# Kernel tuning notes

Measured on AMD Instinct MI355X. Metric: run time of the kernel, lower is better.

## Reference

```python
import jax, jax.numpy as jnp
import numpy as np

EPS = 1e-5

def _bn(x, g, b):
    # training-mode batchnorm over all axes except the last (channel)
    axes = tuple(range(x.ndim - 1))
    m = x.mean(axis=axes, keepdims=True)
    v = x.var(axis=axes, keepdims=True)
    return (x - m) * jax.lax.rsqrt(v + EPS) * g + b

def setup_inputs() -> dict:
    key = jax.random.key(0)
    ks = jax.random.split(key, 9)
    B, N = 4, 4096
    def w(i, shape, fan_in):
        return jax.random.normal(ks[i], shape, jnp.float32) * np.float32(1.0 / np.sqrt(fan_in))
    return {
        "x": jax.random.normal(ks[0], (B, 3, N), jnp.float32),
        "Wq": w(1, (64, 3), 3),
        "Wkv": w(2, (128, 3), 3),
        "Wp1": w(3, (64, 3), 3),
        "Wp2": w(4, (64, 64), 64),
        "Wa": w(5, (64, 64), 64),
        "Wc1": w(6, (64, 64), 64),
        "Wsk": w(7, (64, 6), 6),
        "Wga": w(8, (64, 128), 128),
        "g_p": jnp.ones(64, jnp.float32), "b_p": jnp.zeros(64, jnp.float32),
        "g_a": jnp.ones(64, jnp.float32), "b_a": jnp.zeros(64, jnp.float32),
        "g_c": jnp.ones(64, jnp.float32), "b_c": jnp.zeros(64, jnp.float32),
        "g_sk": jnp.ones(64, jnp.float32), "b_sk": jnp.zeros(64, jnp.float32),
        "g_ga": jnp.ones(64, jnp.float32), "b_ga": jnp.zeros(64, jnp.float32),
        "k": 32,
    }

def reference(x, Wq, Wkv, Wp1, Wp2, Wa, Wc1, Wsk, Wga,
              g_p, b_p, g_a, b_a, g_c, b_c, g_sk, b_sk, g_ga, b_ga, k):
    # x: [B, 3, N] point cloud
    xt = jnp.transpose(x, (0, 2, 1))                      # [B, N, 3]
    B = xt.shape[0]
    # --- KNN neighbor grouping (irregular gather) ---
    sq = jnp.sum(xt * xt, axis=-1)                        # [B, N]
    dist = sq[:, :, None] + sq[:, None, :] - 2.0 * jnp.einsum('bnc,bmc->bnm', xt, xt)
    _, idx = jax.lax.top_k(-dist, k)                      # [B, N, k]
    grouped = xt[jnp.arange(B)[:, None, None], idx]       # [B, N, k, 3]
    rel = grouped - xt[:, :, None, :]                     # relative coords
    # --- local self-attention (1x1 conv QKV + position encoding) ---
    q = jnp.einsum('bnc,dc->bnd', xt, Wq)[:, :, None, :]  # [B, N, 1, 64]
    kv = jnp.einsum('bnkc,dc->bnkd', rel, Wkv)            # [B, N, k, 128]
    kf, vf = kv[..., :64], kv[..., 64:]
    pos = jnp.einsum('bnkd,ed->bnke',
                     jax.nn.relu(_bn(jnp.einsum('bnkc,dc->bnkd', rel, Wp1), g_p, b_p)),
                     Wp2)                                 # [B, N, k, 64]
    logits = jax.nn.relu(_bn(jnp.einsum('bnkd,ed->bnke', q - kf + pos, Wa), g_a, b_a))
    attn = jax.nn.softmax(logits, axis=2)                 # softmax over k neighbors
    agg = jnp.sum(attn * (vf + pos), axis=2)              # [B, N, 64]
    # --- pointnet conv-BN head + skip + fusion ---
    h = jax.nn.relu(_bn(jnp.einsum('bnd,ed->bne', agg, Wc1), g_c, b_c))
    nb_max = jnp.max(grouped, axis=2)                     # [B, N, 3] max-pool over neighbors
    sk = jax.nn.relu(_bn(jnp.einsum('bnc,dc->bnd',
                                    jnp.concatenate([xt, nb_max], axis=-1), Wsk), g_sk, b_sk))
    out = jax.nn.relu(_bn(jnp.einsum('bnc,dc->bnd',
                                     jnp.concatenate([h, sk], axis=-1), Wga), g_ga, b_ga))
    return jnp.transpose(out, (0, 2, 1))                  # [B, 64, N]
```

## Files before the change

### kernel.cpp

```cpp
#include <hip/hip_runtime.h>

#define NBATCH 4
#define NPTS   4096
#define NP     (NBATCH*NPTS)
#define KK     32
#define INF    __builtin_inff()

static const size_t OFF_PTS  = 0;
static const size_t OFF_IDX  = 65536;
static const size_t OFF_TSK  = 589824;
static const size_t OFF_TC   = 1638400;
static const size_t OFF_TGA  = 2686976;
static const size_t OFF_PREL = 3735552;
static const size_t OFF_PSK  = 3735568;
static const size_t OFF_PTA  = 3735696;
static const size_t OFF_PTC  = 3735824;
static const size_t OFF_PTGA = 3735952;
static const size_t OFF_AFF  = 3736080;

typedef __bf16 bf16x8  __attribute__((ext_vector_type(8)));
typedef float  floatx16 __attribute__((ext_vector_type(16)));
#define MFMA32(a,b,c) __builtin_amdgcn_mfma_f32_32x32x16_bf16(a, b, c, 0, 0, 0)

union F8 { bf16x8 v; unsigned short us[8]; uint4 q4; };

__device__ __forceinline__ unsigned short bfbits(float f) {
  unsigned u = __float_as_uint(f);
  return (unsigned short)((u + 0x7FFFu + ((u >> 16) & 1u)) >> 16);
}
__device__ __forceinline__ floatx16 zero16() {
  floatx16 v;
#pragma unroll
  for (int i = 0; i < 16; ++i) v[i] = 0.f;
  return v;
}
__device__ __forceinline__ float wsum(float v) {
#pragma unroll
  for (int o = 32; o; o >>= 1) v += __shfl_xor(v, o, 64);
  return v;
}
__device__ __forceinline__ int isum(int v) {
#pragma unroll
  for (int o = 32; o; o >>= 1) v += __shfl_xor(v, o);
  return v;
}

__global__ __launch_bounds__(256,1) void k_prep(const float* __restrict__ x, float4* __restrict__ pts,
                                                float* __restrict__ pta, float* __restrict__ ptc,
                                                float* __restrict__ ptga, float* __restrict__ prel9,
                                                float* __restrict__ psk128) {
  if (blockIdx.x == 0) {
    if (threadIdx.x < 128) {
      pta[threadIdx.x] = 0.f; ptc[threadIdx.x] = 0.f; ptga[threadIdx.x] = 0.f;
      psk128[threadIdx.x] = 0.f;
    }
    if (threadIdx.x < 16) prel9[threadIdx.x] = 0.f;
  }
  int g = blockIdx.x * 256 + threadIdx.x;
  int b = g / NPTS, n = g % NPTS;
  float vx = x[(b*3+0)*NPTS + n];
  float vy = x[(b*3+1)*NPTS + n];
  float vz = x[(b*3+2)*NPTS + n];
  pts[g] = make_float4(vx, vy, vz, vx*vx + vy*vy + vz*vz);
}

__global__ __launch_bounds__(256) void k_knn(const float4* __restrict__ pts, int* __restrict__ idx,
                                             const float* __restrict__ Wsk, float* __restrict__ tsk,
                                             float* __restrict__ prel9, float* __restrict__ psk128) {
  __shared__ int ocnt[4];
  __shared__ int lsel[128];
  __shared__ float rsum[9], psum[64], pss[64];
  const int tid  = threadIdx.x;
  const int w    = tid >> 6;
  const int lane = tid & 63;
  if (tid < 9)  rsum[tid] = 0.f;
  if (tid < 64) { psum[tid] = 0.f; pss[tid] = 0.f; }
  __syncthreads();
  const int n = blockIdx.x * 4 + w;
  const int batch = n >> 12;
  const float4* base = pts + batch * NPTS;
  const float4 me = pts[n];
  const float wk0 = Wsk[lane*6+0], wk1 = Wsk[lane*6+1], wk2 = Wsk[lane*6+2],
              wk3 = Wsk[lane*6+3], wk4 = Wsk[lane*6+4], wk5 = Wsk[lane*6+5];

  unsigned t0 = 0xFFFFFFFFu, t1 = 0xFFFFFFFFu, t2 = 0xFFFFFFFFu,
           t3 = 0xFFFFFFFFu, t4 = 0xFFFFFFFFu, t5 = 0xFFFFFFFFu;
#pragma unroll 4
  for (int j = 0; j < 64; ++j) {
    float4 p = base[j*64 + lane];
    float dot = fmaf(me.x, p.x, fmaf(me.y, p.y, me.z * p.z));
    float d = fmaxf(fmaf(-2.f, dot, me.w + p.w), 0.f);
    unsigned m = __float_as_uint(d), x;
    x = min(t0, m); m = max(t0, m); t0 = x;
    x = min(t1, m); m = max(t1, m); t1 = x;
    x = min(t2, m); m = max(t2, m); t2 = x;
    x = min(t3, m); m = max(t3, m); t3 = x;
    x = min(t4, m); m = max(t4, m); t4 = x;
    t5 = min(t5, m);
  }

  unsigned glo = t0, ghi = t5;
#pragma unroll
  for (int o = 32; o; o >>= 1) {
    glo = min(glo, (unsigned)__shfl_xor((int)glo, o));
    ghi = max(ghi, (unsigned)__shfl_xor((int)ghi, o));
  }

  unsigned lo = glo, hi = ghi, tau = ghi;
  bool exact = false;
  while (lo < hi) {
    unsigned mid = lo + ((hi - lo) >> 1);
    int c = (t0 <= mid) + (t1 <= mid) + (t2 <= mid) +
            (t3 <= mid) + (t4 <= mid) + (t5 <= mid);
    c = isum(c);
    if (c == 32) { tau = mid; exact = true; break; }
    if (c > 32) hi = mid; else lo = mid + 1;
  }
  if (!exact) tau = lo;

  if (__ballot(t5 <= tau) != 0ull) {
    lo = glo; hi = tau; exact = false;
    while (lo < hi) {
      unsigned mid = lo + ((hi - lo) >> 1);
      int c = 0;
      for (int j = 0; j < 64; ++j) {
        float4 p = base[j*64 + lane];
        float dot = fmaf(me.x, p.x, fmaf(me.y, p.y, me.z * p.z));
        float d = fmaxf(fmaf(-2.f, dot, me.w + p.w), 0.f);
        c += (__float_as_uint(d) <= mid) ? 1 : 0;
      }
      c = isum(c);
      if (c == 32) { tau = mid; exact = true; break; }
      if (c > 32) hi = mid; else lo = mid + 1;
    }
    if (!exact) tau = lo;
  }

  if (lane == 0) ocnt[w] = 0;
  int* op = idx + n * KK;
  unsigned long long em = 0;
#pragma unroll 4
  for (int j = 0; j < 64; ++j) {
    float4 p = base[j*64 + lane];
    float dot = fmaf(me.x, p.x, fmaf(me.y, p.y, me.z * p.z));
    float d = fmaxf(fmaf(-2.f, dot, me.w + p.w), 0.f);
    unsigned k = __float_as_uint(d);
    bool take = exact ? (k <= tau) : (k < tau);
    if (take) {
      int s = atomicAdd(&ocnt[w], 1);
      int m = j*64 + lane;
      if (s < KK) { op[s] = m; lsel[w*32 + s] = m; }
    }
    if (k == tau) em |= 1ull << j;
  }
  if (!exact) {
    int n1 = ocnt[w];
    int need = KK - n1;
    for (int f = 0; f < need; ++f) {
      int myj = em ? (int)__builtin_ctzll(em) : 64;
      int mym = (myj < 64) ? (myj*64 + lane) : 0x7FFFFFFF;
      int g = mym;
#pragma unroll
      for (int o = 32; o; o >>= 1) g = min(g, __shfl_xor(g, o));
      if (mym == g && myj < 64) { em &= em - 1; op[n1 + f] = mym; lsel[w*32 + n1 + f] = mym; }
    }
  }

  int mi = lsel[w*32 + (lane & 31)];
  float4 p = base[mi];
  bool act = lane < 32;
  float r0 = act ? p.x - me.x : 0.f;
  float r1 = act ? p.y - me.y : 0.f;
  float r2 = act ? p.z - me.z : 0.f;
  float vals[9] = { r0, r1, r2, r0*r0, r0*r1, r0*r2, r1*r1, r1*r2, r2*r2 };
#pragma unroll
  for (int t = 0; t < 9; ++t) {
    float rs = wsum(vals[t]);
    if (lane == 0) atomicAdd(&rsum[t], rs);
  }
  float nx = act ? p.x : -INF, ny = act ? p.y : -INF, nz = act ? p.z : -INF;
#pragma unroll
  for (int o = 32; o; o >>= 1) {
    nx = fmaxf(nx, __shfl_xor(nx, o));
    ny = fmaxf(ny, __shfl_xor(ny, o));
    nz = fmaxf(nz, __shfl_xor(nz, o));
  }
  float ts = fmaf(me.x, wk0, fmaf(me.y, wk1, fmaf(me.z, wk2,
             fmaf(nx, wk3, fmaf(ny, wk4, nz * wk5)))));
  tsk[n*64 + lane] = ts;
  atomicAdd(&psum[lane], ts);
  atomicAdd(&pss[lane], ts * ts);
  __syncthreads();
  if (tid < 9)  atomicAdd(&prel9[tid], rsum[tid]);
  if (tid < 64) atomicAdd(&psk128[tid], psum[tid]);
  else if (tid < 128) atomicAdd(&psk128[tid], pss[tid - 64]);
}

__global__ __launch_bounds__(64,1) void k_fin1(const float* __restrict__ prel9, const float* __restrict__ psk128,
                                               const float* __restrict__ Wp1,
                                               const float* __restrict__ g_p, const float* __restrict__ b_p,
                                               const float* __restrict__ g_sk, const float* __restrict__ b_sk,
                                               float* __restrict__ aff) {
  int d = threadIdx.x;
  double C = (double)NP * (double)KK;
  double mr0 = prel9[0]/C, mr1 = prel9[1]/C, mr2 = prel9[2]/C;
  double e00 = prel9[3]/C, e01 = prel9[4]/C, e02 = prel9[5]/C;
  double e11 = prel9[6]/C, e12 = prel9[7]/C, e22 = prel9[8]/C;
  double w0 = Wp1[d*3+0], w1 = Wp1[d*3+1], w2 = Wp1[d*3+2];
  double mu  = w0*mr0 + w1*mr1 + w2*mr2;
  double ex2 = w0*w0*e00 + w1*w1*e11 + w2*w2*e22 + 2.0*(w0*w1*e01 + w0*w2*e02 + w1*w2*e12);
  double var = ex2 - mu*mu;
  double sc  = (double)g_p[d] / sqrt(var + 1e-5);
  aff[0*64 + d] = (float)sc;
  aff[1*64 + d] = (float)((double)b_p[d] - mu*sc);
  double mean = (double)psk128[d] / (double)NP;
  double v2   = (double)psk128[64+d] / (double)NP - mean*mean;
  double sc4  = (double)g_sk[d] / sqrt(v2 + 1e-5);
  aff[6*64 + d] = (float)sc4;
  aff[7*64 + d] = (float)((double)b_sk[d] - mean*sc4);
}

__global__ __launch_bounds__(64,1) void k_fin2(const float* __restrict__ st, double C,
                                               const float* __restrict__ g, const float* __restrict__ b,
                                               float* __restrict__ s_out, float* __restrict__ o_out) {
  int d = threadIdx.x;
  double mean = (double)st[d] / C;
  double var  = (double)st[64 + d] / C - mean*mean;
  double sc   = (double)g[d] / sqrt(var + 1e-5);
  s_out[d] = (float)sc;
  o_out[d] = (float)((double)b[d] - mean*sc);
}

template<int MODE>
__global__ __launch_bounds__(256,1) void k_entry(const float4* __restrict__ pts, const int* __restrict__ idx,
                                                 const float* __restrict__ Wq, const float* __restrict__ Wkv,
                                                 const float* __restrict__ Wp1, const float* __restrict__ Wp2,
                                                 const float* __restrict__ Wa, const float* __restrict__ Wc1,
                                                 const float* __restrict__ aff, float* __restrict__ pstats,
                                                 float* __restrict__ tc) {
  __shared__ __align__(16) unsigned short ybuf[4][32][72];
  __shared__ __align__(16) float aggbuf[4][64];
  __shared__ float psum[64], pss[64];
  if (threadIdx.x < 64) { psum[threadIdx.x] = 0.f; pss[threadIdx.x] = 0.f; }
  __syncthreads();
  const int lane = threadIdx.x & 63;
  const int w    = threadIdx.x >> 6;
  const int c    = lane & 31;
  const int q5   = lane >> 5;

  F8 B0[2];
#pragma unroll
  for (int nt = 0; nt < 2; ++nt)
#pragma unroll
    for (int t = 0; t < 8; ++t)
      B0[nt].us[t] = (q5 == 0 && t < 3) ? bfbits(Wp1[(nt*32+c)*3 + t]) : (unsigned short)0;

  F8 Bs[4][2], B2[4][2];
#pragma unroll
  for (int kt = 0; kt < 4; ++kt)
#pragma unroll
    for (int h = 0; h < 2; ++h) {
      const float* p2 = Wp2 + (h*32+c)*64 + kt*16 + q5*8;
      float4 a = *(const float4*)p2, b = *(const float4*)(p2 + 4);
      Bs[kt][h].us[0]=bfbits(a.x); Bs[kt][h].us[1]=bfbits(a.y); Bs[kt][h].us[2]=bfbits(a.z); Bs[kt][h].us[3]=bfbits(a.w);
      Bs[kt][h].us[4]=bfbits(b.x); Bs[kt][h].us[5]=bfbits(b.y); Bs[kt][h].us[6]=bfbits(b.z); Bs[kt][h].us[7]=bfbits(b.w);
      const float* pa = Wa + (h*32+c)*64 + kt*16 + q5*8;
      float4 e = *(const float4*)pa, f = *(const float4*)(pa + 4);
      B2[kt][h].us[0]=bfbits(e.x); B2[kt][h].us[1]=bfbits(e.y); B2[kt][h].us[2]=bfbits(e.z); B2[kt][h].us[3]=bfbits(e.w);
      B2[kt][h].us[4]=bfbits(f.x); B2[kt][h].us[5]=bfbits(f.y); B2[kt][h].us[6]=bfbits(f.z); B2[kt][h].us[7]=bfbits(f.w);
    }

  F8 Bk4[4];
#pragma unroll
  for (int nt = 0; nt < 4; ++nt) {
    if (MODE == 0 && nt >= 2) { for (int t = 0; t < 8; ++t) Bk4[nt].us[t] = 0; continue; }
    int e = (nt & 1)*32 + c;
#pragma unroll
    for (int t = 0; t < 8; ++t)
      Bk4[nt].us[t] = (q5 == 0 && t < 3)
        ? bfbits(nt < 2 ? -Wkv[e*3 + t] : Wkv[(64+e)*3 + t]) : (unsigned short)0;
  }

  const float s1a = aff[c],      o1a = aff[64+c];
  const float s1b = aff[32+c],   o1b = aff[96+c];
  float s2a = 0.f, o2a = 0.f, s2b = 0.f, o2b = 0.f;
  if (MODE == 1) { s2a = aff[128+c]; o2a = aff[192+c]; s2b = aff[160+c]; o2b = aff[224+c]; }
  const float wqa0 = Wq[c*3+0],      wqa1 = Wq[c*3+1],      wqa2 = Wq[c*3+2];
  const float wqb0 = Wq[(32+c)*3+0], wqb1 = Wq[(32+c)*3+1], wqb2 = Wq[(32+c)*3+2];

  const int wave_id = blockIdx.x * 4 + w;
  const int n0 = wave_id * 8;
  const int batch = n0 >> 12;
  const float4* base = pts + batch * NPTS;

  for (int pi = 0; pi < 8; ++pi) {
    const int n = n0 + pi;
    const float4 me = pts[n];
    const int nb = idx[n*KK + c];
    const float4 pp = base[nb];
    const float r0 = pp.x - me.x, r1 = pp.y - me.y, r2 = pp.z - me.z;
    F8 relA;
#pragma unroll
    for (int t = 0; t < 8; ++t) relA.us[t] = 0;
    if (q5 == 0) { relA.us[0] = bfbits(r0); relA.us[1] = bfbits(r1); relA.us[2] = bfbits(r2); }

    const floatx16 z = zero16();
    floatx16 y0 = MFMA32(relA.v, B0[0].v, z);
    floatx16 y1 = MFMA32(relA.v, B0[1].v, z);
#pragma unroll
    for (int r = 0; r < 16; ++r) {
      int row = (r & 3) + 8*(r >> 2) + 4*q5;
      ybuf[w][row][c]      = bfbits(fmaxf(fmaf(y0[r], s1a, o1a), 0.f));
      ybuf[w][row][32 + c] = bfbits(fmaxf(fmaf(y1[r], s1b, o1b), 0.f));
    }
    F8 Ay[4];
#pragma unroll
    for (int kt = 0; kt < 4; ++kt) Ay[kt].q4 = *(const uint4*)&ybuf[w][c][kt*16 + q5*8];

    floatx16 Cp0 = z, Cp1 = z;
#pragma unroll
    for (int kt = 0; kt < 4; ++kt) {
      Cp0 = MFMA32(Ay[kt].v, Bs[kt][0].v, Cp0);
      Cp1 = MFMA32(Ay[kt].v, Bs[kt][1].v, Cp1);
    }
    floatx16 Cu0 = MFMA32(relA.v, Bk4[0].v, Cp0);
    floatx16 Cu1 = MFMA32(relA.v, Bk4[1].v, Cp1);
    if (MODE == 1) {
      Cp0 = MFMA32(relA.v, Bk4[2].v, Cp0);
      Cp1 = MFMA32(relA.v, Bk4[3].v, Cp1);
    }
    const float qa = fmaf(me.x, wqa0, fmaf(me.y, wqa1, me.z * wqa2));
    const float qb = fmaf(me.x, wqb0, fmaf(me.y, wqb1, me.z * wqb2));
#pragma unroll
    for (int r = 0; r < 16; ++r) {
      int row = (r & 3) + 8*(r >> 2) + 4*q5;
      ybuf[w][row][c]      = bfbits(Cu0[r] + qa);
      ybuf[w][row][32 + c] = bfbits(Cu1[r] + qb);
    }
    F8 Au[4];
#pragma unroll
    for (int kt = 0; kt < 4; ++kt) Au[kt].q4 = *(const uint4*)&ybuf[w][c][kt*16 + q5*8];
    floatx16 Ct0 = z, Ct1 = z;
#pragma unroll
    for (int kt = 0; kt < 4; ++kt) {
      Ct0 = MFMA32(Au[kt].v, B2[kt][0].v, Ct0);
      Ct1 = MFMA32(Au[kt].v, B2[kt][1].v, Ct1);
    }

    if (MODE == 0) {
      float sa = 0.f, qqa = 0.f, sb = 0.f, qqb = 0.f;
#pragma unroll
      for (int r = 0; r < 16; ++r) {
        sa += Ct0[r]; qqa = fmaf(Ct0[r], Ct0[r], qqa);
        sb += Ct1[r]; qqb = fmaf(Ct1[r], Ct1[r], qqb);
      }
      sa += __shfl_xor(sa, 32); qqa += __shfl_xor(qqa, 32);
      sb += __shfl_xor(sb, 32); qqb += __shfl_xor(qqb, 32);
      if (q5 == 0) {
        atomicAdd(&psum[c], sa);      atomicAdd(&pss[c], qqa);
        atomicAdd(&psum[32+c], sb);   atomicAdd(&pss[32+c], qqb);
      }
    } else {
      float ma = -INF, mb = -INF;
#pragma unroll
      for (int r = 0; r < 16; ++r) {
        float la = fmaxf(fmaf(Ct0[r], s2a, o2a), 0.f); Ct0[r] = la; ma = fmaxf(ma, la);
        float lb = fmaxf(fmaf(Ct1[r], s2b, o2b), 0.f); Ct1[r] = lb; mb = fmaxf(mb, lb);
      }
      ma = fmaxf(ma, __shfl_xor(ma, 32));
      mb = fmaxf(mb, __shfl_xor(mb, 32));
      float sa = 0.f, sb = 0.f, aga = 0.f, agb = 0.f;
#pragma unroll
      for (int r = 0; r < 16; ++r) {
        float ta = __expf(Ct0[r] - ma); sa += ta; aga = fmaf(ta, Cp0[r], aga);
        float tb = __expf(Ct1[r] - mb); sb += tb; agb = fmaf(tb, Cp1[r], agb);
      }
      sa += __shfl_xor(sa, 32); aga += __shfl_xor(aga, 32);
      sb += __shfl_xor(sb, 32); agb += __shfl_xor(agb, 32);
      if (q5 == 0) {
        aggbuf[w][c]      = aga / sa;
        aggbuf[w][32 + c] = agb / sb;
      }
      float acc = 0.f;
#pragma unroll
      for (int g = 0; g < 16; ++g) {
        float4 av = *(const float4*)&aggbuf[w][g*4];
        const float4 wv = *(const float4*)(Wc1 + lane*64 + g*4);
        acc = fmaf(av.x, wv.x, fmaf(av.y, wv.y, fmaf(av.z, wv.z, fmaf(av.w, wv.w, acc))));
      }
      tc[n*64 + lane] = acc;
      atomicAdd(&psum[lane], acc);
      atomicAdd(&pss[lane], acc * acc);
    }
  }
  __syncthreads();
  if (threadIdx.x < 64) atomicAdd(&pstats[threadIdx.x], psum[threadIdx.x]);
  else if (threadIdx.x < 128) atomicAdd(&pstats[threadIdx.x], pss[threadIdx.x - 64]);
}

__global__ __launch_bounds__(256,1) void k_final(const float* __restrict__ tcb, const float* __restrict__ tskb,
                                                 const float* __restrict__ Wga, const float* __restrict__ aff,
                                                 float* __restrict__ tga, float* __restrict__ pstats) {
  __shared__ __align__(16) float hb[4][64];
  __shared__ __align__(16) float sb[4][64];
  __shared__ float psum[64], pss[64];
  if (threadIdx.x < 64) { psum[threadIdx.x] = 0.f; pss[threadIdx.x] = 0.f; }
  __syncthreads();
  const int lane = threadIdx.x & 63;
  const int w    = threadIdx.x >> 6;
  const int n = blockIdx.x * 4 + w;
  hb[w][lane] = fmaxf(fmaf(tcb[n*64 + lane],  aff[256 + lane], aff[320 + lane]), 0.f);
  sb[w][lane] = fmaxf(fmaf(tskb[n*64 + lane], aff[384 + lane], aff[448 + lane]), 0.f);
  float g0=0,g1=0,g2=0,g3=0;
#pragma unroll
  for (int d = 0; d < 64; d += 4) {
    const float4 hv = *(const float4*)&hb[w][d];
    const float4 wg = *(const float4*)(Wga + lane*128 + d);
    g0 = fmaf(hv.x, wg.x, g0);
    g1 = fmaf(hv.y, wg.y, g1);
    g2 = fmaf(hv.z, wg.z, g2);
    g3 = fmaf(hv.w, wg.w, g3);
  }
#pragma unroll
  for (int d = 0; d < 64; d += 4) {
    const float4 sv = *(const float4*)&sb[w][d];
    const float4 wg = *(const float4*)(Wga + lane*128 + 64 + d);
    g0 = fmaf(sv.x, wg.x, g0);
    g1 = fmaf(sv.y, wg.y, g1);
    g2 = fmaf(sv.z, wg.z, g2);
    g3 = fmaf(sv.w, wg.w, g3);
  }
  const float tg = (g0+g1) + (g2+g3);
  tga[n*64 + lane] = tg;
  atomicAdd(&psum[lane], tg);
  atomicAdd(&pss[lane], tg * tg);
  __syncthreads();
  if (threadIdx.x < 64) atomicAdd(&pstats[threadIdx.x], psum[threadIdx.x]);
  else if (threadIdx.x < 128) atomicAdd(&pstats[threadIdx.x], pss[threadIdx.x - 64]);
}

__global__ __launch_bounds__(256,1) void k_out(const float* __restrict__ tga, const float* __restrict__ aff,
                                               float* __restrict__ out) {
  int g = blockIdx.x * 256 + threadIdx.x;
  int nn = g & 4095;
  int e  = (g >> 12) & 63;
  int b  = g >> 18;
  float v = tga[((b << 12) + nn) * 64 + e];
  out[g] = fmaxf(fmaf(v, aff[512 + e], aff[576 + e]), 0.f);
}

extern "C" void kernel_launch(void* const* d_in, const int* in_sizes, int n_in,
                              void* d_out, int out_size, void* d_ws, size_t ws_size,
                              hipStream_t stream) {
  const float* x    = (const float*)d_in[0];
  const float* Wq   = (const float*)d_in[1];
  const float* Wkv  = (const float*)d_in[2];
  const float* Wp1  = (const float*)d_in[3];
  const float* Wp2  = (const float*)d_in[4];
  const float* Wa   = (const float*)d_in[5];
  const float* Wc1  = (const float*)d_in[6];
  const float* Wsk  = (const float*)d_in[7];
  const float* Wga  = (const float*)d_in[8];
  const float* g_p  = (const float*)d_in[9];
  const float* b_p  = (const float*)d_in[10];
  const float* g_a  = (const float*)d_in[11];
  const float* b_a  = (const float*)d_in[12];
  const float* g_c  = (const float*)d_in[13];
  const float* b_c  = (const float*)d_in[14];
  const float* g_sk = (const float*)d_in[15];
  const float* b_sk = (const float*)d_in[16];
  const float* g_ga = (const float*)d_in[17];
  const float* b_ga = (const float*)d_in[18];
  float* W = (float*)d_ws;
  float4*  pts   = (float4*)(W + OFF_PTS);
  int*     idx   = (int*)(W + OFF_IDX);
  float*   tsk   = W + OFF_TSK;
  float*   tc    = W + OFF_TC;
  float*   tga   = W + OFF_TGA;
  float*   prel9 = W + OFF_PREL;
  float*   psk   = W + OFF_PSK;
  float*   pta   = W + OFF_PTA;
  float*   ptc   = W + OFF_PTC;
  float*   ptga  = W + OFF_PTGA;
  float*   aff   = W + OFF_AFF;
  float*   out   = (float*)d_out;

  k_prep<<<64, 256, 0, stream>>>(x, pts, pta, ptc, ptga, prel9, psk);
  k_knn<<<4096, 256, 0, stream>>>(pts, idx, Wsk, tsk, prel9, psk);
  k_fin1<<<1, 64, 0, stream>>>(prel9, psk, Wp1, g_p, b_p, g_sk, b_sk, aff);
  k_entry<0><<<512, 256, 0, stream>>>(pts, idx, Wq, Wkv, Wp1, Wp2, Wa, nullptr, aff, pta, nullptr);
  k_fin2<<<1, 64, 0, stream>>>(pta, (double)NP * (double)KK, g_a, b_a, aff + 128, aff + 192);
  k_entry<1><<<512, 256, 0, stream>>>(pts, idx, Wq, Wkv, Wp1, Wp2, Wa, Wc1, aff, ptc, tc);
  k_fin2<<<1, 64, 0, stream>>>(ptc, (double)NP, g_c, b_c, aff + 256, aff + 320);
  k_final<<<4096, 256, 0, stream>>>(tc, tsk, Wga, aff, tga, ptga);
  k_fin2<<<1, 64, 0, stream>>>(ptga, (double)NP, g_ga, b_ga, aff + 512, aff + 576);
  k_out<<<4096, 256, 0, stream>>>(tga, aff, out);
}
```

Measured before the change: 489.0 us.

## Fuse BN finalize kernels via last-block counters, track KNN indices, widen entry grid

Removes the four single-block finalize kernels by having the last block of each producer kernel, detected with a global atomic counter, compute the batchnorm affine parameters. KNN now keeps candidate indices alongside the per-lane top-6 distances, so when all neighbors fit in registers it skips the rescan over all points. The entry kernels process 2 points per wave instead of 8, with the grid quadrupled to 2048 blocks. Costs are extra fences and atomics at each block's end, and more registers in the KNN insertion network.

Result: slower. 1.163 ms (+137.9%).

```diff
diff --git a/kernel.cpp b/kernel.cpp
--- a/kernel.cpp
+++ b/kernel.cpp
@@ -17,6 +17,7 @@
 static const size_t OFF_PTC  = 3735824;
 static const size_t OFF_PTGA = 3735952;
 static const size_t OFF_AFF  = 3736080;
+static const size_t OFF_CNT  = 3736720;
 
 typedef __bf16 bf16x8  __attribute__((ext_vector_type(8)));
 typedef float  floatx16 __attribute__((ext_vector_type(16)));
@@ -44,17 +45,28 @@
   for (int o = 32; o; o >>= 1) v += __shfl_xor(v, o);
   return v;
 }
+__device__ __forceinline__ float aread(float* p) { return atomicAdd(p, 0.f); }
+
+__device__ __forceinline__ void fin2_body(float* st, double C, const float* g, const float* b,
+                                          float* s_out, float* o_out, int d) {
+  double mean = (double)aread(st + d) / C;
+  double var  = (double)aread(st + 64 + d) / C - mean*mean;
+  double sc   = (double)g[d] / sqrt(var + 1e-5);
+  s_out[d] = (float)sc;
+  o_out[d] = (float)((double)b[d] - mean*sc);
+}
 
 __global__ __launch_bounds__(256,1) void k_prep(const float* __restrict__ x, float4* __restrict__ pts,
                                                 float* __restrict__ pta, float* __restrict__ ptc,
                                                 float* __restrict__ ptga, float* __restrict__ prel9,
-                                                float* __restrict__ psk128) {
+                                                float* __restrict__ psk128, unsigned* __restrict__ cnt) {
   if (blockIdx.x == 0) {
     if (threadIdx.x < 128) {
       pta[threadIdx.x] = 0.f; ptc[threadIdx.x] = 0.f; ptga[threadIdx.x] = 0.f;
       psk128[threadIdx.x] = 0.f;
     }
     if (threadIdx.x < 16) prel9[threadIdx.x] = 0.f;
+    if (threadIdx.x < 4)  cnt[threadIdx.x] = 0u;
   }
   int g = blockIdx.x * 256 + threadIdx.x;
   int b = g / NPTS, n = g % NPTS;
@@ -66,10 +78,16 @@
 
 __global__ __launch_bounds__(256) void k_knn(const float4* __restrict__ pts, int* __restrict__ idx,
                                              const float* __restrict__ Wsk, float* __restrict__ tsk,
-                                             float* __restrict__ prel9, float* __restrict__ psk128) {
+                                             float* __restrict__ prel9, float* __restrict__ psk128,
+                                             unsigned* __restrict__ gcnt,
+                                             const float* __restrict__ Wp1,
+                                             const float* __restrict__ g_p, const float* __restrict__ b_p,
+                                             const float* __restrict__ g_sk, const float* __restrict__ b_sk,
+                                             float* __restrict__ aff) {
   __shared__ int ocnt[4];
   __shared__ int lsel[128];
   __shared__ float rsum[9], psum[64], pss[64];
+  __shared__ int amlast;
   const int tid  = threadIdx.x;
   const int w    = tid >> 6;
   const int lane = tid & 63;
@@ -83,23 +101,26 @@
   const float wk0 = Wsk[lane*6+0], wk1 = Wsk[lane*6+1], wk2 = Wsk[lane*6+2],
               wk3 = Wsk[lane*6+3], wk4 = Wsk[lane*6+4], wk5 = Wsk[lane*6+5];
 
-  unsigned t0 = 0xFFFFFFFFu, t1 = 0xFFFFFFFFu, t2 = 0xFFFFFFFFu,
-           t3 = 0xFFFFFFFFu, t4 = 0xFFFFFFFFu, t5 = 0xFFFFFFFFu;
+  unsigned ka[6]; int ia[6];
+#pragma unroll
+  for (int r = 0; r < 6; ++r) { ka[r] = 0xFFFFFFFFu; ia[r] = 0; }
 #pragma unroll 4
   for (int j = 0; j < 64; ++j) {
     float4 p = base[j*64 + lane];
     float dot = fmaf(me.x, p.x, fmaf(me.y, p.y, me.z * p.z));
     float d = fmaxf(fmaf(-2.f, dot, me.w + p.w), 0.f);
-    unsigned m = __float_as_uint(d), x;
-    x = min(t0, m); m = max(t0, m); t0 = x;
-    x = min(t1, m); m = max(t1, m); t1 = x;
-    x = min(t2, m); m = max(t2, m); t2 = x;
-    x = min(t3, m); m = max(t3, m); t3 = x;
-    x = min(t4, m); m = max(t4, m); t4 = x;
-    t5 = min(t5, m);
-  }
-
-  unsigned glo = t0, ghi = t5;
+    unsigned k = __float_as_uint(d);
+    int id = j*64 + lane;
+#pragma unroll
+    for (int r = 0; r < 6; ++r) {
+      bool c = k < ka[r];
+      unsigned tk = c ? ka[r] : k; int ti = c ? ia[r] : id;
+      ka[r] = c ? k : ka[r];       ia[r] = c ? id : ia[r];
+      k = tk; id = ti;
+    }
+  }
+
+  unsigned glo = ka[0], ghi = ka[5];
 #pragma unroll
   for (int o = 32; o; o >>= 1) {
     glo = min(glo, (unsigned)__shfl_xor((int)glo, o));
@@ -110,16 +131,43 @@
   bool exact = false;
   while (lo < hi) {
     unsigned mid = lo + ((hi - lo) >> 1);
-    int c = (t0 <= mid) + (t1 <= mid) + (t2 <= mid) +
-            (t3 <= mid) + (t4 <= mid) + (t5 <= mid);
+    int c = (ka[0] <= mid) + (ka[1] <= mid) + (ka[2] <= mid) +
+            (ka[3] <= mid) + (ka[4] <= mid) + (ka[5] <= mid);
     c = isum(c);
     if (c == 32) { tau = mid; exact = true; break; }
     if (c > 32) hi = mid; else lo = mid + 1;
   }
   if (!exact) tau = lo;
 
-  if (__ballot(t5 <= tau) != 0ull) {
-    lo = glo; hi = tau; exact = false;
+  if (lane == 0) ocnt[w] = 0;
+  int* op = idx + n * KK;
+
+  if (__ballot(ka[5] <= tau) == 0ull) {
+#pragma unroll
+    for (int r = 0; r < 6; ++r) {
+      bool take = exact ? (ka[r] <= tau) : (ka[r] < tau);
+      if (take) {
+        int s = atomicAdd(&ocnt[w], 1);
+        op[s] = ia[r]; lsel[w*32 + s] = ia[r];
+      }
+    }
+    if (!exact) {
+      unsigned used = 0;
+      int n1 = ocnt[w];
+      int need = KK - n1;
+      for (int f = 0; f < need; ++f) {
+        int my = 0x7FFFFFFF, which = -1;
+#pragma unroll
+        for (int r = 0; r < 6; ++r)
+          if (!((used >> r) & 1) && ka[r] == tau && ia[r] < my) { my = ia[r]; which = r; }
+        int g = my;
+#pragma unroll
+        for (int o = 32; o; o >>= 1) g = min(g, __shfl_xor(g, o));
+        if (my == g && which >= 0) { used |= 1u << which; op[n1 + f] = my; lsel[w*32 + n1 + f] = my; }
+      }
+    }
+  } else {
+    lo = glo; hi = ghi; tau = ghi; exact = false;
     while (lo < hi) {
       unsigned mid = lo + ((hi - lo) >> 1);
       int c = 0;
@@ -134,35 +182,31 @@
       if (c > 32) hi = mid; else lo = mid + 1;
     }
     if (!exact) tau = lo;
-  }
-
-  if (lane == 0) ocnt[w] = 0;
-  int* op = idx + n * KK;
-  unsigned long long em = 0;
-#pragma unroll 4
-  for (int j = 0; j < 64; ++j) {
-    float4 p = base[j*64 + lane];
-    float dot = fmaf(me.x, p.x, fmaf(me.y, p.y, me.z * p.z));
-    float d = fmaxf(fmaf(-2.f, dot, me.w + p.w), 0.f);
-    unsigned k = __float_as_uint(d);
-    bool take = exact ? (k <= tau) : (k < tau);
-    if (take) {
-      int s = atomicAdd(&ocnt[w], 1);
-      int m = j*64 + lane;
-      if (s < KK) { op[s] = m; lsel[w*32 + s] = m; }
-    }
-    if (k == tau) em |= 1ull << j;
-  }
-  if (!exact) {
-    int n1 = ocnt[w];
-    int need = KK - n1;
-    for (int f = 0; f < need; ++f) {
-      int myj = em ? (int)__builtin_ctzll(em) : 64;
-      int mym = (myj < 64) ? (myj*64 + lane) : 0x7FFFFFFF;
-      int g = mym;
-#pragma unroll
-      for (int o = 32; o; o >>= 1) g = min(g, __shfl_xor(g, o));
-      if (mym == g && myj < 64) { em &= em - 1; op[n1 + f] = mym; lsel[w*32 + n1 + f] = mym; }
+    unsigned long long em = 0;
+    for (int j = 0; j < 64; ++j) {
+      float4 p = base[j*64 + lane];
+      float dot = fmaf(me.x, p.x, fmaf(me.y, p.y, me.z * p.z));
+      float d = fmaxf(fmaf(-2.f, dot, me.w + p.w), 0.f);
+      unsigned k = __float_as_uint(d);
+      bool take = exact ? (k <= tau) : (k < tau);
+      if (take) {
+        int s = atomicAdd(&ocnt[w], 1);
+        int m = j*64 + lane;
+        if (s < KK) { op[s] = m; lsel[w*32 + s] = m; }
+      }
+      if (k == tau) em |= 1ull << j;
+    }
+    if (!exact) {
+      int n1 = ocnt[w];
+      int need = KK - n1;
+      for (int f = 0; f < need; ++f) {
+        int myj = em ? (int)__builtin_ctzll(em) : 64;
+        int mym = (myj < 64) ? (myj*64 + lane) : 0x7FFFFFFF;
+        int g = mym;
+#pragma unroll
+        for (int o = 32; o; o >>= 1) g = min(g, __shfl_xor(g, o));
+        if (mym == g && myj < 64) { em &= em - 1; op[n1 + f] = mym; lsel[w*32 + n1 + f] = mym; }
+      }
     }
   }
 
@@ -194,41 +238,26 @@
   if (tid < 9)  atomicAdd(&prel9[tid], rsum[tid]);
   if (tid < 64) atomicAdd(&psk128[tid], psum[tid]);
   else if (tid < 128) atomicAdd(&psk128[tid], pss[tid - 64]);
-}
-
-__global__ __launch_bounds__(64,1) void k_fin1(const float* __restrict__ prel9, const float* __restrict__ psk128,
-                                               const float* __restrict__ Wp1,
-                                               const float* __restrict__ g_p, const float* __restrict__ b_p,
-                                               const float* __restrict__ g_sk, const float* __restrict__ b_sk,
-                                               float* __restrict__ aff) {
-  int d = threadIdx.x;
-  double C = (double)NP * (double)KK;
-  double mr0 = prel9[0]/C, mr1 = prel9[1]/C, mr2 = prel9[2]/C;
-  double e00 = prel9[3]/C, e01 = prel9[4]/C, e02 = prel9[5]/C;
-  double e11 = prel9[6]/C, e12 = prel9[7]/C, e22 = prel9[8]/C;
-  double w0 = Wp1[d*3+0], w1 = Wp1[d*3+1], w2 = Wp1[d*3+2];
-  double mu  = w0*mr0 + w1*mr1 + w2*mr2;
-  double ex2 = w0*w0*e00 + w1*w1*e11 + w2*w2*e22 + 2.0*(w0*w1*e01 + w0*w2*e02 + w1*w2*e12);
-  double var = ex2 - mu*mu;
-  double sc  = (double)g_p[d] / sqrt(var + 1e-5);
-  aff[0*64 + d] = (float)sc;
-  aff[1*64 + d] = (float)((double)b_p[d] - mu*sc);
-  double mean = (double)psk128[d] / (double)NP;
-  double v2   = (double)psk128[64+d] / (double)NP - mean*mean;
-  double sc4  = (double)g_sk[d] / sqrt(v2 + 1e-5);
-  aff[6*64 + d] = (float)sc4;
-  aff[7*64 + d] = (float)((double)b_sk[d] - mean*sc4);
-}
-
-__global__ __launch_bounds__(64,1) void k_fin2(const float* __restrict__ st, double C,
-                                               const float* __restrict__ g, const float* __restrict__ b,
-                                               float* __restrict__ s_out, float* __restrict__ o_out) {
-  int d = threadIdx.x;
-  double mean = (double)st[d] / C;
-  double var  = (double)st[64 + d] / C - mean*mean;
-  double sc   = (double)g[d] / sqrt(var + 1e-5);
-  s_out[d] = (float)sc;
-  o_out[d] = (float)((double)b[d] - mean*sc);
+
+  __threadfence();
+  __syncthreads();
+  if (tid == 0) amlast = (atomicAdd(gcnt, 1u) == 4096u - 1u);
+  __syncthreads();
+  if (amlast && tid < 64) {
+    int d = tid;
+    double C = (double)NP * (double)KK;
+    double mr0 = aread(prel9+0)/C, mr1 = aread(prel9+1)/C, mr2 = aread(prel9+2)/C;
+    double e00 = aread(prel9+3)/C, e01 = aread(prel9+4)/C, e02 = aread(prel9+5)/C;
+    double e11 = aread(prel9+6)/C, e12 = aread(prel9+7)/C, e22 = aread(prel9+8)/C;
+    double w0 = Wp1[d*3+0], w1 = Wp1[d*3+1], w2 = Wp1[d*3+2];
+    double mu  = w0*mr0 + w1*mr1 + w2*mr2;
+    double ex2 = w0*w0*e00 + w1*w1*e11 + w2*w2*e22 + 2.0*(w0*w1*e01 + w0*w2*e02 + w1*w2*e12);
+    double var = ex2 - mu*mu;
+    double sc  = (double)g_p[d] / sqrt(var + 1e-5);
+    aff[0*64 + d] = (float)sc;
+    aff[1*64 + d] = (float)((double)b_p[d] - mu*sc);
+    fin2_body(psk128, (double)NP, g_sk, b_sk, aff + 384, aff + 448, d);
+  }
 }
 
 template<int MODE>
@@ -236,11 +265,13 @@
                                                  const float* __restrict__ Wq, const float* __restrict__ Wkv,
                                                  const float* __restrict__ Wp1, const float* __restrict__ Wp2,
                                                  const float* __restrict__ Wa, const float* __restrict__ Wc1,
-                                                 const float* __restrict__ aff, float* __restrict__ pstats,
-                                                 float* __restrict__ tc) {
+                                                 float* __restrict__ aff, float* __restrict__ pstats,
+                                                 float* __restrict__ tc, unsigned* __restrict__ gcnt,
+                                                 const float* __restrict__ gg, const float* __restrict__ bb) {
   __shared__ __align__(16) unsigned short ybuf[4][32][72];
   __shared__ __align__(16) float aggbuf[4][64];
   __shared__ float psum[64], pss[64];
+  __shared__ int amlast;
   if (threadIdx.x < 64) { psum[threadIdx.x] = 0.f; pss[threadIdx.x] = 0.f; }
   __syncthreads();
   const int lane = threadIdx.x & 63;
@@ -289,11 +320,11 @@
   const float wqb0 = Wq[(32+c)*3+0], wqb1 = Wq[(32+c)*3+1], wqb2 = Wq[(32+c)*3+2];
 
   const int wave_id = blockIdx.x * 4 + w;
-  const int n0 = wave_id * 8;
+  const int n0 = wave_id * 2;
   const int batch = n0 >> 12;
   const float4* base = pts + batch * NPTS;
 
-  for (int pi = 0; pi < 8; ++pi) {
+  for (int pi = 0; pi < 2; ++pi) {
     const int n = n0 + pi;
     const float4 me = pts[n];
     const int nb = idx[n*KK + c];
@@ -396,14 +427,28 @@
   __syncthreads();
   if (threadIdx.x < 64) atomicAdd(&pstats[threadIdx.x], psum[threadIdx.x]);
   else if (threadIdx.x < 128) atomicAdd(&pstats[threadIdx.x], pss[threadIdx.x - 64]);
+
+  __threadfence();
+  __syncthreads();
+  if (threadIdx.x == 0) amlast = (atomicAdd(gcnt, 1u) == 2048u - 1u);
+  __syncthreads();
+  if (amlast && threadIdx.x < 64) {
+    double C = (MODE == 0) ? (double)NP * (double)KK : (double)NP;
+    float* s_out = (MODE == 0) ? aff + 128 : aff + 256;
+    float* o_out = (MODE == 0) ? aff + 192 : aff + 320;
+    fin2_body(pstats, C, gg, bb, s_out, o_out, threadIdx.x);
+  }
 }
 
 __global__ __launch_bounds__(256,1) void k_final(const float* __restrict__ tcb, const float* __restrict__ tskb,
-                                                 const float* __restrict__ Wga, const float* __restrict__ aff,
-                                                 float* __restrict__ tga, float* __restrict__ pstats) {
+                                                 const float* __restrict__ Wga, float* __restrict__ aff,
+                                                 float* __restrict__ tga, float* __restrict__ pstats,
+                                                 unsigned* __restrict__ gcnt,
+                                                 const float* __restrict__ g_ga, const float* __restrict__ b_ga) {
   __shared__ __align__(16) float hb[4][64];
   __shared__ __align__(16) float sb[4][64];
   __shared__ float psum[64], pss[64];
+  __shared__ int amlast;
   if (threadIdx.x < 64) { psum[threadIdx.x] = 0.f; pss[threadIdx.x] = 0.f; }
   __syncthreads();
   const int lane = threadIdx.x & 63;
@@ -437,6 +482,12 @@
   __syncthreads();
   if (threadIdx.x < 64) atomicAdd(&pstats[threadIdx.x], psum[threadIdx.x]);
   else if (threadIdx.x < 128) atomicAdd(&pstats[threadIdx.x], pss[threadIdx.x - 64]);
+  __threadfence();
+  __syncthreads();
+  if (threadIdx.x == 0) amlast = (atomicAdd(gcnt, 1u) == 4096u - 1u);
+  __syncthreads();
+  if (amlast && threadIdx.x < 64)
+    fin2_body(pstats, (double)NP, g_ga, b_ga, aff + 512, aff + 576, threadIdx.x);
 }
 
 __global__ __launch_bounds__(256,1) void k_out(const float* __restrict__ tga, const float* __restrict__ aff,
@@ -472,27 +523,27 @@
   const float* g_ga = (const float*)d_in[17];
   const float* b_ga = (const float*)d_in[18];
   float* W = (float*)d_ws;
-  float4*  pts   = (float4*)(W + OFF_PTS);
-  int*     idx   = (int*)(W + OFF_IDX);
-  float*   tsk   = W + OFF_TSK;
-  float*   tc    = W + OFF_TC;
-  float*   tga   = W + OFF_TGA;
-  float*   prel9 = W + OFF_PREL;
-  float*   psk   = W + OFF_PSK;
-  float*   pta   = W + OFF_PTA;
-  float*   ptc   = W + OFF_PTC;
-  float*   ptga  = W + OFF_PTGA;
-  float*   aff   = W + OFF_AFF;
-  float*   out   = (float*)d_out;
-
-  k_prep<<<64, 256, 0, stream>>>(x, pts, pta, ptc, ptga, prel9, psk);
-  k_knn<<<4096, 256, 0, stream>>>(pts, idx, Wsk, tsk, prel9, psk);
-  k_fin1<<<1, 64, 0, stream>>>(prel9, psk, Wp1, g_p, b_p, g_sk, b_sk, aff);
-  k_entry<0><<<512, 256, 0, stream>>>(pts, idx, Wq, Wkv, Wp1, Wp2, Wa, nullptr, aff, pta, nullptr);
-  k_fin2<<<1, 64, 0, stream>>>(pta, (double)NP * (double)KK, g_a, b_a, aff + 128, aff + 192);
-  k_entry<1><<<512, 256, 0, stream>>>(pts, idx, Wq, Wkv, Wp1, Wp2, Wa, Wc1, aff, ptc, tc);
-  k_fin2<<<1, 64, 0, stream>>>(ptc, (double)NP, g_c, b_c, aff + 256, aff + 320);
-  k_final<<<4096, 256, 0, stream>>>(tc, tsk, Wga, aff, tga, ptga);
-  k_fin2<<<1, 64, 0, stream>>>(ptga, (double)NP, g_ga, b_ga, aff + 512, aff + 576);
+  float4*   pts   = (float4*)(W + OFF_PTS);
+  int*      idx   = (int*)(W + OFF_IDX);
+  float*    tsk   = W + OFF_TSK;
+  float*    tc    = W + OFF_TC;
+  float*    tga   = W + OFF_TGA;
+  float*    prel9 = W + OFF_PREL;
+  float*    psk   = W + OFF_PSK;
+  float*    pta   = W + OFF_PTA;
+  float*    ptc   = W + OFF_PTC;
+  float*    ptga  = W + OFF_PTGA;
+  float*    aff   = W + OFF_AFF;
+  unsigned* cnt   = (unsigned*)(W + OFF_CNT);
+  float*    out   = (float*)d_out;
+
+  k_prep<<<64, 256, 0, stream>>>(x, pts, pta, ptc, ptga, prel9, psk, cnt);
+  k_knn<<<4096, 256, 0, stream>>>(pts, idx, Wsk, tsk, prel9, psk, cnt + 0,
+                                  Wp1, g_p, b_p, g_sk, b_sk, aff);
+  k_entry<0><<<2048, 256, 0, stream>>>(pts, idx, Wq, Wkv, Wp1, Wp2, Wa, nullptr,
+                                       aff, pta, nullptr, cnt + 1, g_a, b_a);
+  k_entry<1><<<2048, 256, 0, stream>>>(pts, idx, Wq, Wkv, Wp1, Wp2, Wa, Wc1,
+                                       aff, ptc, tc, cnt + 2, g_c, b_c);
+  k_final<<<4096, 256, 0, stream>>>(tc, tsk, Wga, aff, tga, ptga, cnt + 3, g_ga, b_ga);
   k_out<<<4096, 256, 0, stream>>>(tga, aff, out);
 }
```
